# Kernel optimization log

Hardware: AMD Instinct MI355X
Metric: run time of the kernel (lower is better)

## Reference

```python
import jax, jax.numpy as jnp
import numpy as np

# Wrapped Conv2D config (channels_last): input 32x32x32 -> output 32x32x64, 3x3 'same', stride 1
H, W, C_IN, C_OUT = 32, 32, 32, 64


def _propagate(w, b, kernel, bias):
    # w: [B, H*W*C_OUT, n_out], b: [B, n_out]
    B, _, n_out = w.shape
    # transpose(0,2,1) + reshape to [B, n_out, H, W, C_OUT]
    wt = jnp.transpose(w, (0, 2, 1)).reshape(B, n_out, H, W, C_OUT)
    # bias-sum reduction: sum over (h, w, c) of w * bias[c], added to b
    b_new = jnp.einsum('bnhwc,c->bn', wt, bias) + b
    # Batched transposed conv over all n_out slices at once (replaces K.rnn loop)
    z = wt.reshape(B * n_out, H, W, C_OUT)
    w_in = jax.lax.conv_transpose(
        z, kernel, strides=(1, 1), padding='SAME',
        dimension_numbers=('NHWC', 'HWIO', 'NHWC'), transpose_kernel=True)
    # -> [B*n_out, H, W, C_IN]; flatten and transpose back to [B, n_in, n_out]
    w_new = jnp.transpose(w_in.reshape(B, n_out, H * W * C_IN), (0, 2, 1))
    return w_new, b_new


def setup_inputs() -> dict:
    key = jax.random.key(0)
    ks = jax.random.split(key, 6)
    B, n_out = 8, 32
    n_flat = H * W * C_OUT
    return {
        'w_out_u': jax.random.normal(ks[0], (B, n_flat, n_out), jnp.float32),
        'b_out_u': jax.random.normal(ks[1], (B, n_out), jnp.float32),
        'w_out_l': jax.random.normal(ks[2], (B, n_flat, n_out), jnp.float32),
        'b_out_l': jax.random.normal(ks[3], (B, n_out), jnp.float32),
        'kernel': jax.random.normal(ks[4], (3, 3, C_IN, C_OUT), jnp.float32) * 0.1,
        'bias': jax.random.normal(ks[5], (C_OUT,), jnp.float32) * 0.1,
    }


def reference(w_out_u, b_out_u, w_out_l, b_out_l, kernel, bias):
    w_u, b_u = _propagate(w_out_u, b_out_u, kernel, bias)
    w_l, b_l = _propagate(w_out_l, b_out_l, kernel, bias)
    return (w_u, b_u, w_l, b_l)
```

## Files before the change

### kernel.cpp

```cpp
#include <hip/hip_runtime.h>
#include <hip/hip_bf16.h>

#define H  32
#define W  32
#define CI 32
#define CO 64
#define NB 8
#define NOUT 32

#define WU_OFF 0
#define BU_OFF (NB * H * W * CI * NOUT)
#define WL_OFF (BU_OFF + NB * NOUT)
#define BL_OFF (WL_OFF + NB * H * W * CI * NOUT)

#define KF_UINT4 2304
#define BP_OFF_BYTES 36864
#define T_OFF_BYTES  65536
#define T_SIDE_BYTES (NB * 1024 * 2048 * 2)

typedef __bf16 bf16x8 __attribute__((ext_vector_type(8)));
typedef float  f32x4  __attribute__((ext_vector_type(4)));

__device__ __forceinline__ unsigned int pack_bf16(float lo, float hi) {
    unsigned int ulo = __float_as_uint(lo) + 0x8000u;
    unsigned int uhi = __float_as_uint(hi) + 0x8000u;
    return (uhi & 0xffff0000u) | (ulo >> 16);
}

__global__ void prep_kernel(const float* __restrict__ K,
                            unsigned int* __restrict__ kws,
                            float* __restrict__ bp) {
    int bx = blockIdx.x, t = threadIdx.x;
    if (bx < 9) {
        int g    = bx * 256 + t;
        int tap  = g >> 8;
        int r    = g & 255;
        int i    = r >> 3;
        int og   = r & 7;
        int c    = og >> 2;
        int quad = og & 3;
        int ih   = i >> 4;
        int lane = quad * 16 + (i & 15);
        int dst  = ((tap * 4 + c * 2 + ih) * 64 + lane) * 4;
        const float4* src = (const float4*)(K + (size_t)g * 8);
        float4 f0 = src[0];
        float4 f1 = src[1];
        kws[dst + 0] = pack_bf16(f0.x, f0.y);
        kws[dst + 1] = pack_bf16(f0.z, f0.w);
        kws[dst + 2] = pack_bf16(f1.x, f1.y);
        kws[dst + 3] = pack_bf16(f1.z, f1.w);
    } else {
        bp[(bx - 9) * 256 + t] = 0.f;
    }
}

__global__ __launch_bounds__(256)
void transpose_kernel(const float* __restrict__ in0,
                      const float* __restrict__ in1,
                      uint4* __restrict__ Tb0,
                      uint4* __restrict__ Tb1,
                      const float* __restrict__ bias,
                      float* __restrict__ bp) {
    __shared__ float bias_s[CO];
    __shared__ float bred[8][32];
    int t = threadIdx.x;
    if (t < CO) bias_s[t] = bias[t];
    __syncthreads();

    int blk  = blockIdx.x;
    int side = blk >> 13;
    int rem  = blk & 8191;
    int b    = rem >> 10;
    int pos  = rem & 1023;
    const float* p = (side ? in1 : in0) + ((size_t)b * 1024 + pos) * 2048;
    uint4* T = side ? Tb1 : Tb0;
    int n  = t & 31;
    int og = t >> 5;
    int o0 = og * 8;

    float v[8];
#pragma unroll
    for (int j = 0; j < 8; j++)
        v[j] = p[(o0 + j) * NOUT + n];

    float s = 0.f;
#pragma unroll
    for (int j = 0; j < 8; j++)
        s = fmaf(v[j], bias_s[o0 + j], s);

    uint4 u;
    u.x = pack_bf16(v[0], v[1]);
    u.y = pack_bf16(v[2], v[3]);
    u.z = pack_bf16(v[4], v[5]);
    u.w = pack_bf16(v[6], v[7]);
    T[((size_t)b * 1024 + pos) * 256 + t] = u;

    bred[og][n] = s;
    __syncthreads();
    if (t < 32) {
        float ss = 0.f;
#pragma unroll
        for (int g = 0; g < 8; g++) ss += bred[g][t];
        atomicAdd(&bp[side * 256 + b * 32 + t], ss);
    }
}

__global__ __launch_bounds__(256, 4)
void conv_t_kernel(const uint4* __restrict__ Tb0,
                   const uint4* __restrict__ Tb1,
                   const uint4* __restrict__ kws,
                   float* __restrict__ out0,
                   float* __restrict__ out1) {
    __shared__ uint4 kf[KF_UINT4];
    int t = threadIdx.x;
#pragma unroll
    for (int k = 0; k < 9; k++) kf[t + 256 * k] = kws[t + 256 * k];
    __syncthreads();

    int bx   = blockIdx.x;
    int side = bx >> 11;
    int rem  = bx & 2047;
    int b    = rem >> 8;
    int slot = rem & 255;
    int h    = slot >> 3;
    int wq   = slot & 7;
    int wave = t >> 6;
    int lane = t & 63;
    int w    = wq * 4 + wave;
    int n16  = lane & 15;
    int quad = lane >> 4;

    const uint4* Tb = (side ? Tb1 : Tb0) + (size_t)b * 1024 * 256;
    f32x4 acc[2][2] = {};
    const bf16x8* kfp = (const bf16x8*)kf;

#pragma unroll
    for (int kh = 0; kh < 3; kh++) {
        int hi = h + 1 - kh;
        if (hi < 0 || hi >= H) continue;
#pragma unroll
        for (int kw = 0; kw < 3; kw++) {
            int wi = w + 1 - kw;
            if (wi < 0 || wi >= W) continue;
            int tap = kh * 3 + kw;
            const uint4* Tp = Tb + (size_t)(hi * W + wi) * 256;
#pragma unroll
            for (int c = 0; c < 2; c++) {
                union { uint4 u; bf16x8 v; } b0, b1;
                b0.u = Tp[(c * 4 + quad) * 32 + n16];
                b1.u = Tp[(c * 4 + quad) * 32 + n16 + 16];
                bf16x8 a0 = kfp[(tap * 4 + c * 2 + 0) * 64 + lane];
                bf16x8 a1 = kfp[(tap * 4 + c * 2 + 1) * 64 + lane];
                acc[0][0] = __builtin_amdgcn_mfma_f32_16x16x32_bf16(a0, b0.v, acc[0][0], 0, 0, 0);
                acc[0][1] = __builtin_amdgcn_mfma_f32_16x16x32_bf16(a0, b1.v, acc[0][1], 0, 0, 0);
                acc[1][0] = __builtin_amdgcn_mfma_f32_16x16x32_bf16(a1, b0.v, acc[1][0], 0, 0, 0);
                acc[1][1] = __builtin_amdgcn_mfma_f32_16x16x32_bf16(a1, b1.v, acc[1][1], 0, 0, 0);
            }
        }
    }

    float* wout = (side ? out1 : out0)
                + (size_t)b * (H * W * CI * NOUT)
                + (size_t)((h * W + w) * CI) * NOUT;
#pragma unroll
    for (int ih = 0; ih < 2; ih++)
#pragma unroll
        for (int nh = 0; nh < 2; nh++)
#pragma unroll
            for (int r = 0; r < 4; r++) {
                int i = ih * 16 + quad * 4 + r;
                int n = nh * 16 + n16;
                wout[i * NOUT + n] = acc[ih][nh][r];
            }
}

__global__ void bias_final32_kernel(const float* __restrict__ bp,
                                    const float* __restrict__ bu,
                                    const float* __restrict__ bl,
                                    float* __restrict__ out) {
    int sb = blockIdx.x;
    int t  = threadIdx.x;
    if (t >= NOUT) return;
    int side = sb >> 3, b = sb & 7;
    const float* bb = side ? bl : bu;
    out[(side ? BL_OFF : BU_OFF) + b * NOUT + t] =
        bb[b * NOUT + t] + bp[sb * 32 + t];
}

__global__ __launch_bounds__(256, 4)
void conv_bwd_kernel(const float* __restrict__ wu,
                     const float* __restrict__ wl,
                     const uint4* __restrict__ kws,
                     float* __restrict__ out) {
    __shared__ uint4 kf[KF_UINT4];
    int t = threadIdx.x;
#pragma unroll
    for (int k = 0; k < 9; k++) kf[t + 256 * k] = kws[t + 256 * k];
    __syncthreads();

    int bx   = blockIdx.x;
    int side = bx >> 11;
    int rem  = bx & 2047;
    int b    = rem >> 8;
    int slot = rem & 255;
    int h    = slot >> 3;
    int wq   = slot & 7;
    int wave = t >> 6;
    int lane = t & 63;
    int w    = wq * 4 + wave;
    int n16  = lane & 15;
    int quad = lane >> 4;

    const float* in  = side ? wl : wu;
    const float* inb = in + (size_t)b * (H * W * CO * NOUT);
    f32x4 acc[2][2] = {};
    const bf16x8* kfp = (const bf16x8*)kf;

#pragma unroll
    for (int kh = 0; kh < 3; kh++) {
        int hi = h + 1 - kh;
        if (hi < 0 || hi >= H) continue;
#pragma unroll
        for (int kw = 0; kw < 3; kw++) {
            int wi = w + 1 - kw;
            if (wi < 0 || wi >= W) continue;
            int tap = kh * 3 + kw;
            const float* p = inb + (size_t)((hi * W + wi) * CO) * NOUT;
#pragma unroll
            for (int c = 0; c < 2; c++) {
                int ob = c * 32 + quad * 8;
                const float* p0 = p + ob * NOUT + n16;
                float v0[8], v1[8];
#pragma unroll
                for (int j = 0; j < 8; j++) {
                    v0[j] = p0[j * NOUT];
                    v1[j] = p0[j * NOUT + 16];
                }
                union { unsigned int u[4]; bf16x8 v; } b0, b1;
#pragma unroll
                for (int j = 0; j < 4; j++) {
                    b0.u[j] = pack_bf16(v0[2 * j], v0[2 * j + 1]);
                    b1.u[j] = pack_bf16(v1[2 * j], v1[2 * j + 1]);
                }
                bf16x8 a0 = kfp[(tap * 4 + c * 2 + 0) * 64 + lane];
                bf16x8 a1 = kfp[(tap * 4 + c * 2 + 1) * 64 + lane];
                acc[0][0] = __builtin_amdgcn_mfma_f32_16x16x32_bf16(a0, b0.v, acc[0][0], 0, 0, 0);
                acc[0][1] = __builtin_amdgcn_mfma_f32_16x16x32_bf16(a0, b1.v, acc[0][1], 0, 0, 0);
                acc[1][0] = __builtin_amdgcn_mfma_f32_16x16x32_bf16(a1, b0.v, acc[1][0], 0, 0, 0);
                acc[1][1] = __builtin_amdgcn_mfma_f32_16x16x32_bf16(a1, b1.v, acc[1][1], 0, 0, 0);
            }
        }
    }

    float* wout = out + (side ? WL_OFF : WU_OFF)
                + (size_t)b * (H * W * CI * NOUT)
                + (size_t)((h * W + w) * CI) * NOUT;
#pragma unroll
    for (int ih = 0; ih < 2; ih++)
#pragma unroll
        for (int nh = 0; nh < 2; nh++)
#pragma unroll
            for (int r = 0; r < 4; r++) {
                int i = ih * 16 + quad * 4 + r;
                int n = nh * 16 + n16;
                wout[i * NOUT + n] = acc[ih][nh][r];
            }
}

__global__ __launch_bounds__(256)
void bias_part_kernel(const float* __restrict__ wu,
                      const float* __restrict__ wl,
                      const float* __restrict__ bias,
                      double* __restrict__ bpart) {
    __shared__ double sred[8][32];
    __shared__ float bias_s[CO];
    int t = threadIdx.x;
    if (t < CO) bias_s[t] = bias[t];
    __syncthreads();

    int blk  = blockIdx.x;
    int sb   = blk >> 5;
    int h    = blk & 31;
    int side = sb >> 3, b = sb & 7;
    const float* in = (side ? wl : wu)
                    + (size_t)b * (H * W * CO * NOUT)
                    + (size_t)h * (W * CO * NOUT);
    int lane = t & 31;
    int g    = t >> 5;
    double acc = 0.0;
    for (int f = g; f < W * CO; f += 8)
        acc += (double)in[(size_t)f * NOUT + lane] * (double)bias_s[f & 63];
    sred[g][lane] = acc;
    __syncthreads();
    if (t < 32) {
        double s = 0.0;
#pragma unroll
        for (int g2 = 0; g2 < 8; g2++) s += sred[g2][t];
        bpart[(size_t)blk * 32 + t] = s;
    }
}

__global__ void bias_final64_kernel(const double* __restrict__ bpart,
                                    const float* __restrict__ bu,
                                    const float* __restrict__ bl,
                                    float* __restrict__ out) {
    int sb = blockIdx.x;
    int t  = threadIdx.x;
    if (t >= NOUT) return;
    double s = 0.0;
    for (int h = 0; h < 32; h++) s += bpart[(size_t)(sb * 32 + h) * 32 + t];
    int side = sb >> 3, b = sb & 7;
    const float* bb = side ? bl : bu;
    out[(side ? BL_OFF : BU_OFF) + b * NOUT + t] =
        (float)((double)bb[b * NOUT + t] + s);
}

extern "C" void kernel_launch(void* const* d_in, const int* in_sizes, int n_in,
                              void* d_out, int out_size, void* d_ws, size_t ws_size,
                              hipStream_t stream) {
    const float* wu   = (const float*)d_in[0];
    const float* bu   = (const float*)d_in[1];
    const float* wl   = (const float*)d_in[2];
    const float* bl   = (const float*)d_in[3];
    const float* K    = (const float*)d_in[4];
    const float* bias = (const float*)d_in[5];
    float* out = (float*)d_out;
    unsigned int* kws = (unsigned int*)d_ws;
    float*  bp    = (float*)((char*)d_ws + BP_OFF_BYTES);
    double* bpart = (double*)((char*)d_ws + BP_OFF_BYTES);
    uint4*  T0    = (uint4*)((char*)d_ws + T_OFF_BYTES);
    uint4*  T1    = (uint4*)((char*)d_ws + T_OFF_BYTES + T_SIDE_BYTES);

    const size_t full_need = (size_t)T_OFF_BYTES + 2 * (size_t)T_SIDE_BYTES;
    const size_t half_need = (size_t)T_OFF_BYTES + (size_t)T_SIDE_BYTES;

    prep_kernel<<<dim3(11), dim3(256), 0, stream>>>(K, kws, bp);

    if (ws_size >= full_need) {
        transpose_kernel<<<dim3(16384), dim3(256), 0, stream>>>(wu, wl, T0, T1, bias, bp);
        conv_t_kernel<<<dim3(4096), dim3(256), 0, stream>>>(T0, T1, (const uint4*)d_ws,
                                                            out + WU_OFF, out + WL_OFF);
        bias_final32_kernel<<<dim3(16), dim3(64), 0, stream>>>(bp, bu, bl, out);
    } else if (ws_size >= half_need) {
        transpose_kernel<<<dim3(8192), dim3(256), 0, stream>>>(wu, wu, T0, T0, bias, bp);
        conv_t_kernel<<<dim3(2048), dim3(256), 0, stream>>>(T0, T0, (const uint4*)d_ws,
                                                            out + WU_OFF, out + WU_OFF);
        transpose_kernel<<<dim3(8192), dim3(256), 0, stream>>>(wl, wl, T0, T0, bias, bp + 256);
        conv_t_kernel<<<dim3(2048), dim3(256), 0, stream>>>(T0, T0, (const uint4*)d_ws,
                                                            out + WL_OFF, out + WL_OFF);
        bias_final32_kernel<<<dim3(16), dim3(64), 0, stream>>>(bp, bu, bl, out);
    } else {
        conv_bwd_kernel<<<dim3(4096), dim3(256), 0, stream>>>(wu, wl, (const uint4*)d_ws, out);
        bias_part_kernel<<<dim3(512), dim3(256), 0, stream>>>(wu, wl, bias, bpart);
        bias_final64_kernel<<<dim3(16), dim3(64), 0, stream>>>(bpart, bu, bl, out);
    }
}
```

Measured before the change: 247.1 us.

## Vectorize transpose loads, stage through swizzled LDS, remap conv block order

The transpose kernel now has each wave handle one spatial position. Threads read float4 vectors instead of strided scalar loads, pack to bf16, and stage through a swizzled shared-memory buffer so global stores stay coalesced. The bias-sum reduction now uses wave shuffles, and the grid shrinks by four because each block covers four positions. The conv kernel's block index is remapped to interleave batch/side combos across the low bits, likely to spread work across XCDs or L2 slices for better cache locality.

```diff
diff --git a/kernel.cpp b/kernel.cpp
--- a/kernel.cpp
+++ b/kernel.cpp
@@ -62,45 +62,75 @@
                       const float* __restrict__ bias,
                       float* __restrict__ bp) {
     __shared__ float bias_s[CO];
-    __shared__ float bred[8][32];
+    __shared__ uint4 stg[4][256];
+    __shared__ float bredf[4 * 32];
     int t = threadIdx.x;
     if (t < CO) bias_s[t] = bias[t];
     __syncthreads();
 
     int blk  = blockIdx.x;
-    int side = blk >> 13;
-    int rem  = blk & 8191;
-    int b    = rem >> 10;
-    int pos  = rem & 1023;
+    int side = blk >> 11;
+    int rem  = blk & 2047;
+    int b    = rem >> 8;
+    int p4   = rem & 255;
+    int wave = t >> 6;
+    int lane = t & 63;
+    int pos  = p4 * 4 + wave;
+    int og   = lane >> 3;
+    int n4   = lane & 7;
+
     const float* p = (side ? in1 : in0) + ((size_t)b * 1024 + pos) * 2048;
-    uint4* T = side ? Tb1 : Tb0;
-    int n  = t & 31;
-    int og = t >> 5;
-    int o0 = og * 8;
-
-    float v[8];
-#pragma unroll
-    for (int j = 0; j < 8; j++)
-        v[j] = p[(o0 + j) * NOUT + n];
-
-    float s = 0.f;
-#pragma unroll
-    for (int j = 0; j < 8; j++)
-        s = fmaf(v[j], bias_s[o0 + j], s);
-
-    uint4 u;
-    u.x = pack_bf16(v[0], v[1]);
-    u.y = pack_bf16(v[2], v[3]);
-    u.z = pack_bf16(v[4], v[5]);
-    u.w = pack_bf16(v[6], v[7]);
-    T[((size_t)b * 1024 + pos) * 256 + t] = u;
-
-    bred[og][n] = s;
-    __syncthreads();
+    const float4* src = (const float4*)(p + og * 256 + n4 * 4);
+
+    float v[8][4];
+#pragma unroll
+    for (int j = 0; j < 8; j++) {
+        float4 f = src[j * 8];
+        v[j][0] = f.x; v[j][1] = f.y; v[j][2] = f.z; v[j][3] = f.w;
+    }
+
+    float s[4] = {0.f, 0.f, 0.f, 0.f};
+#pragma unroll
+    for (int j = 0; j < 8; j++) {
+        float bj = bias_s[og * 8 + j];
+#pragma unroll
+        for (int k = 0; k < 4; k++)
+            s[k] = fmaf(v[j][k], bj, s[k]);
+    }
+
+#pragma unroll
+    for (int k = 0; k < 4; k++) {
+        uint4 u;
+        u.x = pack_bf16(v[0][k], v[1][k]);
+        u.y = pack_bf16(v[2][k], v[3][k]);
+        u.z = pack_bf16(v[4][k], v[5][k]);
+        u.w = pack_bf16(v[6][k], v[7][k]);
+        stg[wave][og * 32 + k * 8 + (n4 ^ og)] = u;
+    }
+
+#pragma unroll
+    for (int off = 8; off < 64; off <<= 1)
+#pragma unroll
+        for (int k = 0; k < 4; k++)
+            s[k] += __shfl_xor(s[k], off, 64);
+    if (lane < 8) {
+#pragma unroll
+        for (int k = 0; k < 4; k++)
+            bredf[wave * 32 + n4 * 4 + k] = s[k];
+    }
+    __syncthreads();
+
+    uint4* T = (side ? Tb1 : Tb0) + ((size_t)b * 1024 + p4 * 4) * 256;
+#pragma unroll
+    for (int q = 0; q < 4; q++) {
+        int g   = q * 64 + lane;
+        int ogr = g >> 5;
+        int nr  = g & 31;
+        T[wave * 256 + g] = stg[wave][ogr * 32 + (nr & 3) * 8 + ((nr >> 2) ^ ogr)];
+    }
+
     if (t < 32) {
-        float ss = 0.f;
-#pragma unroll
-        for (int g = 0; g < 8; g++) ss += bred[g][t];
+        float ss = bredf[t] + bredf[32 + t] + bredf[64 + t] + bredf[96 + t];
         atomicAdd(&bp[side * 256 + b * 32 + t], ss);
     }
 }
@@ -118,10 +148,13 @@
     __syncthreads();
 
     int bx   = blockIdx.x;
-    int side = bx >> 11;
-    int rem  = bx & 2047;
-    int b    = rem >> 8;
-    int slot = rem & 255;
+    int x    = bx & 7;
+    int q    = bx >> 3;
+    int cpx  = gridDim.x >> 11;
+    int combo = x * cpx + (q >> 8);
+    int slot  = q & 255;
+    int side = combo >> 3;
+    int b    = combo & 7;
     int h    = slot >> 3;
     int wq   = slot & 7;
     int wave = t >> 6;
@@ -337,15 +370,15 @@
     prep_kernel<<<dim3(11), dim3(256), 0, stream>>>(K, kws, bp);
 
     if (ws_size >= full_need) {
-        transpose_kernel<<<dim3(16384), dim3(256), 0, stream>>>(wu, wl, T0, T1, bias, bp);
+        transpose_kernel<<<dim3(4096), dim3(256), 0, stream>>>(wu, wl, T0, T1, bias, bp);
         conv_t_kernel<<<dim3(4096), dim3(256), 0, stream>>>(T0, T1, (const uint4*)d_ws,
                                                             out + WU_OFF, out + WL_OFF);
         bias_final32_kernel<<<dim3(16), dim3(64), 0, stream>>>(bp, bu, bl, out);
     } else if (ws_size >= half_need) {
-        transpose_kernel<<<dim3(8192), dim3(256), 0, stream>>>(wu, wu, T0, T0, bias, bp);
+        transpose_kernel<<<dim3(2048), dim3(256), 0, stream>>>(wu, wu, T0, T0, bias, bp);
         conv_t_kernel<<<dim3(2048), dim3(256), 0, stream>>>(T0, T0, (const uint4*)d_ws,
                                                             out + WU_OFF, out + WU_OFF);
-        transpose_kernel<<<dim3(8192), dim3(256), 0, stream>>>(wl, wl, T0, T0, bias, bp + 256);
+        transpose_kernel<<<dim3(2048), dim3(256), 0, stream>>>(wl, wl, T0, T0, bias, bp + 256);
         conv_t_kernel<<<dim3(2048), dim3(256), 0, stream>>>(T0, T0, (const uint4*)d_ws,
                                                             out + WL_OFF, out + WL_OFF);
         bias_final32_kernel<<<dim3(16), dim3(64), 0, stream>>>(bp, bu, bl, out);
```

After: 219.6 us. 11.1% less time.

## Fuse transpose/bf16 pack into conv kernel using shared-memory halo staging

Applied to the files above, without the earlier changes.

Replaces the separate transpose kernel, which wrote a bf16 intermediate buffer to global memory, and the conv kernel that read it back, with one fused kernel. Each block loads a 3x18 spatial halo tile of fp32 input per channel half, packs it to bf16 into swizzled LDS, accumulates the bias reduction on the fly, then runs MFMA over 16 output columns. The goal is to drop the global round trip of the intermediate and one launch. In exchange the halo tiles are reloaded redundantly and the larger LDS footprint lowers occupancy. The workspace-size fallback paths are removed as well.

```diff
diff --git a/kernel.cpp b/kernel.cpp
--- a/kernel.cpp
+++ b/kernel.cpp
@@ -15,8 +15,6 @@
 
 #define KF_UINT4 2304
 #define BP_OFF_BYTES 36864
-#define T_OFF_BYTES  65536
-#define T_SIDE_BYTES (NB * 1024 * 2048 * 2)
 
 typedef __bf16 bf16x8 __attribute__((ext_vector_type(8)));
 typedef float  f32x4  __attribute__((ext_vector_type(4)));
@@ -54,124 +52,142 @@
     }
 }
 
-__global__ __launch_bounds__(256)
-void transpose_kernel(const float* __restrict__ in0,
-                      const float* __restrict__ in1,
-                      uint4* __restrict__ Tb0,
-                      uint4* __restrict__ Tb1,
-                      const float* __restrict__ bias,
-                      float* __restrict__ bp) {
+__global__ __launch_bounds__(512, 2)
+void fused_conv_kernel(const float* __restrict__ in0,
+                       const float* __restrict__ in1,
+                       const uint4* __restrict__ kws,
+                       const float* __restrict__ bias,
+                       float* __restrict__ bp,
+                       float* __restrict__ out0,
+                       float* __restrict__ out1) {
+    __shared__ uint4 kf[KF_UINT4];
+    __shared__ uint4 stg[3 * 18 * 4 * 32];
     __shared__ float bias_s[CO];
-    __shared__ float bred[8][32];
+
     int t = threadIdx.x;
+    for (int k = t; k < KF_UINT4; k += 512) kf[k] = kws[k];
     if (t < CO) bias_s[t] = bias[t];
-    __syncthreads();
-
-    int blk  = blockIdx.x;
-    int side = blk >> 13;
-    int rem  = blk & 8191;
-    int b    = rem >> 10;
-    int pos  = rem & 1023;
-    const float* p = (side ? in1 : in0) + ((size_t)b * 1024 + pos) * 2048;
-    uint4* T = side ? Tb1 : Tb0;
-    int n  = t & 31;
-    int og = t >> 5;
-    int o0 = og * 8;
-
-    float v[8];
-#pragma unroll
-    for (int j = 0; j < 8; j++)
-        v[j] = p[(o0 + j) * NOUT + n];
-
-    float s = 0.f;
-#pragma unroll
-    for (int j = 0; j < 8; j++)
-        s = fmaf(v[j], bias_s[o0 + j], s);
-
-    uint4 u;
-    u.x = pack_bf16(v[0], v[1]);
-    u.y = pack_bf16(v[2], v[3]);
-    u.z = pack_bf16(v[4], v[5]);
-    u.w = pack_bf16(v[6], v[7]);
-    T[((size_t)b * 1024 + pos) * 256 + t] = u;
-
-    bred[og][n] = s;
-    __syncthreads();
-    if (t < 32) {
-        float ss = 0.f;
-#pragma unroll
-        for (int g = 0; g < 8; g++) ss += bred[g][t];
-        atomicAdd(&bp[side * 256 + b * 32 + t], ss);
-    }
-}
-
-__global__ __launch_bounds__(256, 4)
-void conv_t_kernel(const uint4* __restrict__ Tb0,
-                   const uint4* __restrict__ Tb1,
-                   const uint4* __restrict__ kws,
-                   float* __restrict__ out0,
-                   float* __restrict__ out1) {
-    __shared__ uint4 kf[KF_UINT4];
-    int t = threadIdx.x;
-#pragma unroll
-    for (int k = 0; k < 9; k++) kf[t + 256 * k] = kws[t + 256 * k];
-    __syncthreads();
-
-    int bx   = blockIdx.x;
-    int side = bx >> 11;
-    int rem  = bx & 2047;
-    int b    = rem >> 8;
-    int slot = rem & 255;
-    int h    = slot >> 3;
-    int wq   = slot & 7;
+
+    int bx    = blockIdx.x;
+    int x     = bx & 7;
+    int q     = bx >> 3;
+    int combo = x * 2 + (q >> 6);
+    int idx   = q & 63;
+    int side  = combo >> 3;
+    int b     = combo & 7;
+    int h     = idx >> 1;
+    int wh    = idx & 1;
+
+    const float* inp = (side ? in1 : in0) + (size_t)b * 1024 * 2048;
+
+    int unit = t >> 5;
+    int ogp  = (t >> 3) & 3;
+    int n4   = t & 7;
     int wave = t >> 6;
     int lane = t & 63;
-    int w    = wq * 4 + wave;
     int n16  = lane & 15;
     int quad = lane >> 4;
 
-    const uint4* Tb = (side ? Tb1 : Tb0) + (size_t)b * 1024 * 256;
-    f32x4 acc[2][2] = {};
+    f32x4 acc[2][2][2] = {};
+    float sb[4] = {0.f, 0.f, 0.f, 0.f};
     const bf16x8* kfp = (const bf16x8*)kf;
 
-#pragma unroll
-    for (int kh = 0; kh < 3; kh++) {
-        int hi = h + 1 - kh;
-        if (hi < 0 || hi >= H) continue;
-#pragma unroll
-        for (int kw = 0; kw < 3; kw++) {
-            int wi = w + 1 - kw;
-            if (wi < 0 || wi >= W) continue;
-            int tap = kh * 3 + kw;
-            const uint4* Tp = Tb + (size_t)(hi * W + wi) * 256;
-#pragma unroll
-            for (int c = 0; c < 2; c++) {
-                union { uint4 u; bf16x8 v; } b0, b1;
-                b0.u = Tp[(c * 4 + quad) * 32 + n16];
-                b1.u = Tp[(c * 4 + quad) * 32 + n16 + 16];
-                bf16x8 a0 = kfp[(tap * 4 + c * 2 + 0) * 64 + lane];
-                bf16x8 a1 = kfp[(tap * 4 + c * 2 + 1) * 64 + lane];
-                acc[0][0] = __builtin_amdgcn_mfma_f32_16x16x32_bf16(a0, b0.v, acc[0][0], 0, 0, 0);
-                acc[0][1] = __builtin_amdgcn_mfma_f32_16x16x32_bf16(a0, b1.v, acc[0][1], 0, 0, 0);
-                acc[1][0] = __builtin_amdgcn_mfma_f32_16x16x32_bf16(a1, b0.v, acc[1][0], 0, 0, 0);
-                acc[1][1] = __builtin_amdgcn_mfma_f32_16x16x32_bf16(a1, b1.v, acc[1][1], 0, 0, 0);
+    for (int c = 0; c < 2; c++) {
+        __syncthreads();
+        for (int s = 0; s < 4; s++) {
+            int tile = s * 16 + unit;
+            if (tile >= 54) break;
+            int row = tile / 18;
+            int col = tile - row * 18;
+            int hi  = h - 1 + row;
+            int wi  = wh * 16 - 1 + col;
+            if (hi < 0 || hi >= H || wi < 0 || wi >= W) continue;
+            const float* p = inp + (size_t)(hi * W + wi) * 2048
+                           + c * 1024 + ogp * 256 + n4 * 4;
+            float v[8][4];
+#pragma unroll
+            for (int j = 0; j < 8; j++) {
+                float4 f = *(const float4*)(p + j * 32);
+                v[j][0] = f.x; v[j][1] = f.y; v[j][2] = f.z; v[j][3] = f.w;
+            }
+            if (row == 1 && col >= 1 && col <= 16) {
+#pragma unroll
+                for (int j = 0; j < 8; j++) {
+                    float bj = bias_s[c * 32 + ogp * 8 + j];
+#pragma unroll
+                    for (int k = 0; k < 4; k++)
+                        sb[k] = fmaf(v[j][k], bj, sb[k]);
+                }
+            }
+            uint4* dst = &stg[tile * 128 + ogp * 32];
+#pragma unroll
+            for (int k = 0; k < 4; k++) {
+                uint4 u;
+                u.x = pack_bf16(v[0][k], v[1][k]);
+                u.y = pack_bf16(v[2][k], v[3][k]);
+                u.z = pack_bf16(v[4][k], v[5][k]);
+                u.w = pack_bf16(v[6][k], v[7][k]);
+                dst[(n4 * 4 + k) ^ ogp] = u;
             }
         }
-    }
-
-    float* wout = (side ? out1 : out0)
-                + (size_t)b * (H * W * CI * NOUT)
-                + (size_t)((h * W + w) * CI) * NOUT;
-#pragma unroll
-    for (int ih = 0; ih < 2; ih++)
-#pragma unroll
-        for (int nh = 0; nh < 2; nh++)
-#pragma unroll
-            for (int r = 0; r < 4; r++) {
-                int i = ih * 16 + quad * 4 + r;
-                int n = nh * 16 + n16;
-                wout[i * NOUT + n] = acc[ih][nh][r];
-            }
+        __syncthreads();
+#pragma unroll
+        for (int p2 = 0; p2 < 2; p2++) {
+            int wl = wave * 2 + p2;
+            int w  = wh * 16 + wl;
+#pragma unroll
+            for (int kh = 0; kh < 3; kh++) {
+                int hi = h + 1 - kh;
+                if (hi < 0 || hi >= H) continue;
+                int row = 2 - kh;
+#pragma unroll
+                for (int kw = 0; kw < 3; kw++) {
+                    int wi = w + 1 - kw;
+                    if (wi < 0 || wi >= W) continue;
+                    int col = wl + 2 - kw;
+                    int tap = kh * 3 + kw;
+                    const uint4* Tp = &stg[(row * 18 + col) * 128];
+                    union { uint4 u; bf16x8 v; } b0, b1;
+                    b0.u = Tp[quad * 32 + (n16 ^ quad)];
+                    b1.u = Tp[quad * 32 + (n16 ^ quad) + 16];
+                    bf16x8 a0 = kfp[(tap * 4 + c * 2 + 0) * 64 + lane];
+                    bf16x8 a1 = kfp[(tap * 4 + c * 2 + 1) * 64 + lane];
+                    acc[p2][0][0] = __builtin_amdgcn_mfma_f32_16x16x32_bf16(a0, b0.v, acc[p2][0][0], 0, 0, 0);
+                    acc[p2][0][1] = __builtin_amdgcn_mfma_f32_16x16x32_bf16(a0, b1.v, acc[p2][0][1], 0, 0, 0);
+                    acc[p2][1][0] = __builtin_amdgcn_mfma_f32_16x16x32_bf16(a1, b0.v, acc[p2][1][0], 0, 0, 0);
+                    acc[p2][1][1] = __builtin_amdgcn_mfma_f32_16x16x32_bf16(a1, b1.v, acc[p2][1][1], 0, 0, 0);
+                }
+            }
+        }
+    }
+
+#pragma unroll
+    for (int off = 8; off <= 32; off <<= 1)
+#pragma unroll
+        for (int k = 0; k < 4; k++)
+            sb[k] += __shfl_xor(sb[k], off, 64);
+    if (lane < 8) {
+#pragma unroll
+        for (int k = 0; k < 4; k++)
+            atomicAdd(&bp[side * 256 + b * 32 + n4 * 4 + k], sb[k]);
+    }
+
+    float* outp = (side ? out1 : out0) + (size_t)b * (H * W * CI * NOUT);
+#pragma unroll
+    for (int p2 = 0; p2 < 2; p2++) {
+        int w = wh * 16 + wave * 2 + p2;
+        float* wout = outp + (size_t)((h * W + w) * CI) * NOUT;
+#pragma unroll
+        for (int ih = 0; ih < 2; ih++)
+#pragma unroll
+            for (int nh = 0; nh < 2; nh++)
+#pragma unroll
+                for (int r = 0; r < 4; r++) {
+                    int i = ih * 16 + quad * 4 + r;
+                    int n = nh * 16 + n16;
+                    wout[i * NOUT + n] = acc[p2][ih][nh][r];
+                }
+    }
 }
 
 __global__ void bias_final32_kernel(const float* __restrict__ bp,
@@ -187,134 +203,6 @@
         bb[b * NOUT + t] + bp[sb * 32 + t];
 }
 
-__global__ __launch_bounds__(256, 4)
-void conv_bwd_kernel(const float* __restrict__ wu,
-                     const float* __restrict__ wl,
-                     const uint4* __restrict__ kws,
-                     float* __restrict__ out) {
-    __shared__ uint4 kf[KF_UINT4];
-    int t = threadIdx.x;
-#pragma unroll
-    for (int k = 0; k < 9; k++) kf[t + 256 * k] = kws[t + 256 * k];
-    __syncthreads();
-
-    int bx   = blockIdx.x;
-    int side = bx >> 11;
-    int rem  = bx & 2047;
-    int b    = rem >> 8;
-    int slot = rem & 255;
-    int h    = slot >> 3;
-    int wq   = slot & 7;
-    int wave = t >> 6;
-    int lane = t & 63;
-    int w    = wq * 4 + wave;
-    int n16  = lane & 15;
-    int quad = lane >> 4;
-
-    const float* in  = side ? wl : wu;
-    const float* inb = in + (size_t)b * (H * W * CO * NOUT);
-    f32x4 acc[2][2] = {};
-    const bf16x8* kfp = (const bf16x8*)kf;
-
-#pragma unroll
-    for (int kh = 0; kh < 3; kh++) {
-        int hi = h + 1 - kh;
-        if (hi < 0 || hi >= H) continue;
-#pragma unroll
-        for (int kw = 0; kw < 3; kw++) {
-            int wi = w + 1 - kw;
-            if (wi < 0 || wi >= W) continue;
-            int tap = kh * 3 + kw;
-            const float* p = inb + (size_t)((hi * W + wi) * CO) * NOUT;
-#pragma unroll
-            for (int c = 0; c < 2; c++) {
-                int ob = c * 32 + quad * 8;
-                const float* p0 = p + ob * NOUT + n16;
-                float v0[8], v1[8];
-#pragma unroll
-                for (int j = 0; j < 8; j++) {
-                    v0[j] = p0[j * NOUT];
-                    v1[j] = p0[j * NOUT + 16];
-                }
-                union { unsigned int u[4]; bf16x8 v; } b0, b1;
-#pragma unroll
-                for (int j = 0; j < 4; j++) {
-                    b0.u[j] = pack_bf16(v0[2 * j], v0[2 * j + 1]);
-                    b1.u[j] = pack_bf16(v1[2 * j], v1[2 * j + 1]);
-                }
-                bf16x8 a0 = kfp[(tap * 4 + c * 2 + 0) * 64 + lane];
-                bf16x8 a1 = kfp[(tap * 4 + c * 2 + 1) * 64 + lane];
-                acc[0][0] = __builtin_amdgcn_mfma_f32_16x16x32_bf16(a0, b0.v, acc[0][0], 0, 0, 0);
-                acc[0][1] = __builtin_amdgcn_mfma_f32_16x16x32_bf16(a0, b1.v, acc[0][1], 0, 0, 0);
-                acc[1][0] = __builtin_amdgcn_mfma_f32_16x16x32_bf16(a1, b0.v, acc[1][0], 0, 0, 0);
-                acc[1][1] = __builtin_amdgcn_mfma_f32_16x16x32_bf16(a1, b1.v, acc[1][1], 0, 0, 0);
-            }
-        }
-    }
-
-    float* wout = out + (side ? WL_OFF : WU_OFF)
-                + (size_t)b * (H * W * CI * NOUT)
-                + (size_t)((h * W + w) * CI) * NOUT;
-#pragma unroll
-    for (int ih = 0; ih < 2; ih++)
-#pragma unroll
-        for (int nh = 0; nh < 2; nh++)
-#pragma unroll
-            for (int r = 0; r < 4; r++) {
-                int i = ih * 16 + quad * 4 + r;
-                int n = nh * 16 + n16;
-                wout[i * NOUT + n] = acc[ih][nh][r];
-            }
-}
-
-__global__ __launch_bounds__(256)
-void bias_part_kernel(const float* __restrict__ wu,
-                      const float* __restrict__ wl,
-                      const float* __restrict__ bias,
-                      double* __restrict__ bpart) {
-    __shared__ double sred[8][32];
-    __shared__ float bias_s[CO];
-    int t = threadIdx.x;
-    if (t < CO) bias_s[t] = bias[t];
-    __syncthreads();
-
-    int blk  = blockIdx.x;
-    int sb   = blk >> 5;
-    int h    = blk & 31;
-    int side = sb >> 3, b = sb & 7;
-    const float* in = (side ? wl : wu)
-                    + (size_t)b * (H * W * CO * NOUT)
-                    + (size_t)h * (W * CO * NOUT);
-    int lane = t & 31;
-    int g    = t >> 5;
-    double acc = 0.0;
-    for (int f = g; f < W * CO; f += 8)
-        acc += (double)in[(size_t)f * NOUT + lane] * (double)bias_s[f & 63];
-    sred[g][lane] = acc;
-    __syncthreads();
-    if (t < 32) {
-        double s = 0.0;
-#pragma unroll
-        for (int g2 = 0; g2 < 8; g2++) s += sred[g2][t];
-        bpart[(size_t)blk * 32 + t] = s;
-    }
-}
-
-__global__ void bias_final64_kernel(const double* __restrict__ bpart,
-                                    const float* __restrict__ bu,
-                                    const float* __restrict__ bl,
-                                    float* __restrict__ out) {
-    int sb = blockIdx.x;
-    int t  = threadIdx.x;
-    if (t >= NOUT) return;
-    double s = 0.0;
-    for (int h = 0; h < 32; h++) s += bpart[(size_t)(sb * 32 + h) * 32 + t];
-    int side = sb >> 3, b = sb & 7;
-    const float* bb = side ? bl : bu;
-    out[(side ? BL_OFF : BU_OFF) + b * NOUT + t] =
-        (float)((double)bb[b * NOUT + t] + s);
-}
-
 extern "C" void kernel_launch(void* const* d_in, const int* in_sizes, int n_in,
                               void* d_out, int out_size, void* d_ws, size_t ws_size,
                               hipStream_t stream) {
@@ -326,32 +214,10 @@
     const float* bias = (const float*)d_in[5];
     float* out = (float*)d_out;
     unsigned int* kws = (unsigned int*)d_ws;
-    float*  bp    = (float*)((char*)d_ws + BP_OFF_BYTES);
-    double* bpart = (double*)((char*)d_ws + BP_OFF_BYTES);
-    uint4*  T0    = (uint4*)((char*)d_ws + T_OFF_BYTES);
-    uint4*  T1    = (uint4*)((char*)d_ws + T_OFF_BYTES + T_SIDE_BYTES);
-
-    const size_t full_need = (size_t)T_OFF_BYTES + 2 * (size_t)T_SIDE_BYTES;
-    const size_t half_need = (size_t)T_OFF_BYTES + (size_t)T_SIDE_BYTES;
+    float* bp = (float*)((char*)d_ws + BP_OFF_BYTES);
 
     prep_kernel<<<dim3(11), dim3(256), 0, stream>>>(K, kws, bp);
-
-    if (ws_size >= full_need) {
-        transpose_kernel<<<dim3(16384), dim3(256), 0, stream>>>(wu, wl, T0, T1, bias, bp);
-        conv_t_kernel<<<dim3(4096), dim3(256), 0, stream>>>(T0, T1, (const uint4*)d_ws,
-                                                            out + WU_OFF, out + WL_OFF);
-        bias_final32_kernel<<<dim3(16), dim3(64), 0, stream>>>(bp, bu, bl, out);
-    } else if (ws_size >= half_need) {
-        transpose_kernel<<<dim3(8192), dim3(256), 0, stream>>>(wu, wu, T0, T0, bias, bp);
-        conv_t_kernel<<<dim3(2048), dim3(256), 0, stream>>>(T0, T0, (const uint4*)d_ws,
-                                                            out + WU_OFF, out + WU_OFF);
-        transpose_kernel<<<dim3(8192), dim3(256), 0, stream>>>(wl, wl, T0, T0, bias, bp + 256);
-        conv_t_kernel<<<dim3(2048), dim3(256), 0, stream>>>(T0, T0, (const uint4*)d_ws,
-                                                            out + WL_OFF, out + WL_OFF);
-        bias_final32_kernel<<<dim3(16), dim3(64), 0, stream>>>(bp, bu, bl, out);
-    } else {
-        conv_bwd_kernel<<<dim3(4096), dim3(256), 0, stream>>>(wu, wl, (const uint4*)d_ws, out);
-        bias_part_kernel<<<dim3(512), dim3(256), 0, stream>>>(wu, wl, bias, bpart);
-        bias_final64_kernel<<<dim3(16), dim3(64), 0, stream>>>(bpart, bu, bl, out);
-    }
-}
+    fused_conv_kernel<<<dim3(1024), dim3(512), 0, stream>>>(
+        wu, wl, (const uint4*)d_ws, bias, bp, out + WU_OFF, out + WL_OFF);
+    bias_final32_kernel<<<dim3(16), dim3(64), 0, stream>>>(bp, bu, bl, out);
+}
```

Result: faster. 228.7 us (-7.4%).
